# Performance work log

Measured on AMD Instinct MI355X. Metric: run time of the kernel, lower is better.

Reference implementation:

```python
import jax, jax.numpy as jnp
import numpy as np

EMBED_DIM = 2048
NUM_HEADS = 32
HEAD_DIM = EMBED_DIM // NUM_HEADS
SCALE = HEAD_DIM ** -0.5
B, S = 2, 2048


def setup_inputs() -> dict:
    key = jax.random.key(0)
    ks = jax.random.split(key, 9)
    std = EMBED_DIM ** -0.5
    inp = {
        "h": jax.random.normal(ks[0], (B, S, EMBED_DIM), dtype=jnp.float32),
        "Wq": jax.random.normal(ks[1], (EMBED_DIM, EMBED_DIM), dtype=jnp.float32) * std,
        "bq": jax.random.normal(ks[2], (EMBED_DIM,), dtype=jnp.float32) * 0.02,
        "Wk": jax.random.normal(ks[3], (EMBED_DIM, EMBED_DIM), dtype=jnp.float32) * std,
        "bk": jax.random.normal(ks[4], (EMBED_DIM,), dtype=jnp.float32) * 0.02,
        "Wv": jax.random.normal(ks[5], (EMBED_DIM, EMBED_DIM), dtype=jnp.float32) * std,
        "bv": jax.random.normal(ks[6], (EMBED_DIM,), dtype=jnp.float32) * 0.02,
        "Wo": jax.random.normal(ks[7], (EMBED_DIM, EMBED_DIM), dtype=jnp.float32) * std,
        "bo": jax.random.normal(ks[8], (EMBED_DIM,), dtype=jnp.float32) * 0.02,
    }
    return inp


def reference(h, Wq, bq, Wk, bk, Wv, bv, Wo, bo):
    # QKV projections (nn.Linear: x @ W.T + b)
    q = h @ Wq.T + bq  # [B, S, E]
    k = h @ Wk.T + bk
    v = h @ Wv.T + bv
    # split heads
    q = q.reshape(B, S, NUM_HEADS, HEAD_DIM)
    k = k.reshape(B, S, NUM_HEADS, HEAD_DIM)
    v = v.reshape(B, S, NUM_HEADS, HEAD_DIM)
    # scaled dot-product attention with causal (tril) mask
    scores = jnp.einsum("bqhd,bkhd->bhqk", q, k) * SCALE  # [B, H, S, S]
    causal = jnp.tril(jnp.ones((S, S), dtype=bool))  # [S, S]
    neg = jnp.finfo(scores.dtype).min
    scores = jnp.where(causal[None, None, :, :], scores, neg)
    attn = jax.nn.softmax(scores, axis=-1)
    o = jnp.einsum("bhqk,bkhd->bqhd", attn, v).reshape(B, S, EMBED_DIM)
    return o @ Wo.T + bo
```

## Files before the change

kernel.cpp:

```cpp
#include <hip/hip_runtime.h>
#include <hip/hip_bf16.h>
#include <stdint.h>

#define EMBED 2048
#define NHEADS 32
#define HDIM 64
#define BATCH 2
#define SEQ 2048
#define ATT_SCALE 0.125f
#define LOG2E 1.4426950408889634f

typedef __attribute__((ext_vector_type(8))) short bf16x8;
typedef __attribute__((ext_vector_type(4))) float f32x4;
typedef __attribute__((ext_vector_type(16))) float f32x16;
typedef __attribute__((ext_vector_type(4))) unsigned short u16x4;
typedef __attribute__((ext_vector_type(2))) unsigned int u32x2;

static __device__ __forceinline__ unsigned short f2bf(float f) {
  union { float f; uint32_t u; } v; v.f = f;
  uint32_t r = v.u + 0x7fffu + ((v.u >> 16) & 1u);
  return (unsigned short)(r >> 16);
}

static __device__ __forceinline__ void gload_lds16(const unsigned short* g, unsigned short* l) {
  __builtin_amdgcn_global_load_lds(
      (const __attribute__((address_space(1))) unsigned int*)g,
      (__attribute__((address_space(3))) unsigned int*)l, 16, 0, 0);
}

__global__ void cvt_all(const float* __restrict__ h,
                        const float* __restrict__ Wq, const float* __restrict__ Wk,
                        const float* __restrict__ Wv, const float* __restrict__ Wo,
                        unsigned short* __restrict__ out) {
  const int n4 = 6291456;
  int idx = blockIdx.x * blockDim.x + threadIdx.x;
  int stride = gridDim.x * blockDim.x;
  for (int i = idx; i < n4; i += stride) {
    const float* src; int off;
    if (i < 2097152)      { src = h;  off = i; }
    else if (i < 3145728) { src = Wq; off = i - 2097152; }
    else if (i < 4194304) { src = Wk; off = i - 3145728; }
    else if (i < 5242880) { src = Wv; off = i - 4194304; }
    else                  { src = Wo; off = i - 5242880; }
    float4 v = ((const float4*)src)[off];
    u16x4 o;
    o.x = f2bf(v.x); o.y = f2bf(v.y); o.z = f2bf(v.z); o.w = f2bf(v.w);
    ((u16x4*)out)[i] = o;
  }
}

__global__ __launch_bounds__(512, 2)
void gemm_qkv192(const unsigned short* __restrict__ A,
                 const unsigned short* __restrict__ W,
                 const float* __restrict__ b0, const float* __restrict__ b1,
                 const float* __restrict__ b2,
                 unsigned short* __restrict__ o0, unsigned short* __restrict__ o1,
                 unsigned short* __restrict__ o2, float qscale) {
  __shared__ unsigned short lds[2][28672];
  const int tid = threadIdx.x;
  const int w = tid >> 6, l = tid & 63;
  const int wm = w >> 2, wn = w & 3;
  const int r16 = l & 15, g = l >> 4;
  const int xcd = blockIdx.x & 7, t8 = blockIdx.x >> 3;
  const int bi = (xcd >> 2) * 8 + (t8 & 7);
  const int bj = (xcd & 3) * 8 + (t8 >> 3);
  const int arow0 = bi * 256, bcol0 = bj * 192;

  f32x4 acc[8][3];
#pragma unroll
  for (int i = 0; i < 8; ++i)
#pragma unroll
    for (int j = 0; j < 3; ++j) acc[i][j] = (f32x4){0.f, 0.f, 0.f, 0.f};

  const int lr8 = (l >> 3) & 7;
  const int gcu = ((l & 7) ^ lr8) * 8;

  auto stageA = [&](int buf, int kt, int base) {
    gload_lds16(A + (size_t)(arow0 + base + (tid >> 3)) * 2048 + kt * 64 + gcu,
                &lds[buf][(base + w * 8) * 64]);
  };
  auto stageB = [&](int buf, int kt, int k) {
    gload_lds16(W + (size_t)(bcol0 + k * 64 + (tid >> 3)) * 2048 + kt * 64 + gcu,
                &lds[buf][16384 + (k * 64 + w * 8) * 64]);
  };
  auto ldA = [&](int buf, int mf, int ks) -> bf16x8 {
    const int row = wm * 128 + mf * 16 + r16;
    const int u = (ks * 4 + g) ^ (r16 & 7);
    return *(const bf16x8*)&lds[buf][row * 64 + u * 8];
  };
  auto ldB = [&](int buf, int nf, int ks) -> bf16x8 {
    const int row = wn * 48 + nf * 16 + r16;
    const int u = (ks * 4 + g) ^ (r16 & 7);
    return *(const bf16x8*)&lds[buf][16384 + row * 64 + u * 8];
  };

  bf16x8 af[4][2], bfr[3][2];

#define MMA_H(MH)                                                                  \
  __builtin_amdgcn_s_setprio(1);                                                   \
  _Pragma("unroll")                                                                \
  for (int i = 0; i < 4; ++i)                                                      \
    _Pragma("unroll")                                                              \
    for (int j = 0; j < 3; ++j)                                                    \
      _Pragma("unroll")                                                            \
      for (int ks = 0; ks < 2; ++ks)                                               \
        acc[(MH)*4 + i][j] = __builtin_amdgcn_mfma_f32_16x16x32_bf16(              \
            af[i][ks], bfr[j][ks], acc[(MH)*4 + i][j], 0, 0, 0);                   \
  __builtin_amdgcn_s_setprio(0);

  stageB(0, 0, 0); stageB(0, 0, 1); stageB(0, 0, 2);
  stageA(0, 0, 0); stageA(0, 0, 128);
  stageA(0, 0, 64); stageA(0, 0, 192);
  asm volatile("s_waitcnt vmcnt(2)" ::: "memory");
  __builtin_amdgcn_sched_barrier(0);
  __builtin_amdgcn_s_barrier();

  const int nt = 32;
  for (int c = 0; c < nt; ++c) {
    const int X = c & 1, Y = X ^ 1;
    const bool s1 = (c + 1 < nt);
#pragma unroll
    for (int i = 0; i < 4; ++i) { af[i][0] = ldA(X, i, 0); af[i][1] = ldA(X, i, 1); }
#pragma unroll
    for (int j = 0; j < 3; ++j) { bfr[j][0] = ldB(X, j, 0); bfr[j][1] = ldB(X, j, 1); }
    if (s1) { stageB(Y, c + 1, 0); stageB(Y, c + 1, 1); stageB(Y, c + 1, 2); }
    MMA_H(0);
    __builtin_amdgcn_s_barrier();
    if (s1) asm volatile("s_waitcnt vmcnt(3)" ::: "memory");
    else    asm volatile("s_waitcnt vmcnt(0)" ::: "memory");
    __builtin_amdgcn_sched_barrier(0);
#pragma unroll
    for (int i = 0; i < 4; ++i) { af[i][0] = ldA(X, i + 4, 0); af[i][1] = ldA(X, i + 4, 1); }
    if (s1) {
      stageA(Y, c + 1, 0); stageA(Y, c + 1, 128);
      stageA(Y, c + 1, 64); stageA(Y, c + 1, 192);
    }
    MMA_H(1);
    if (s1) asm volatile("s_waitcnt vmcnt(2)" ::: "memory");
    else    asm volatile("s_waitcnt vmcnt(0)" ::: "memory");
    __builtin_amdgcn_sched_barrier(0);
    __builtin_amdgcn_s_barrier();
  }
#undef MMA_H

#pragma unroll
  for (int mf = 0; mf < 8; ++mf) {
    const int irow = arow0 + wm * 128 + mf * 16 + g * 4;
#pragma unroll
    for (int nf = 0; nf < 3; ++nf) {
      const int jcol = bcol0 + wn * 48 + nf * 16 + r16;
      const int which = jcol >> 11;
      const int jl = jcol & 2047;
      const int hh = jl >> 6, d = jl & 63;
      const float bval = (which == 0) ? b0[jl] : (which == 1) ? b1[jl] : b2[jl];
      const float osc = (which == 0) ? qscale : 1.0f;
      unsigned short* outp = (which == 0) ? o0 : (which == 1) ? o1 : o2;
#pragma unroll
      for (int rr = 0; rr < 4; ++rr) {
        const float val = (acc[mf][nf][rr] + bval) * osc;
        const int i = irow + rr;
        const int b = i >> 11, s = i & 2047;
        size_t off;
        if (which < 2) off = (((size_t)(b * NHEADS + hh)) * SEQ + s) * HDIM + d;
        else           off = (((size_t)(b * NHEADS + hh)) * HDIM + d) * SEQ + s;
        outp[off] = f2bf(val);
      }
    }
  }
}

__global__ __launch_bounds__(512, 2)
void gemm8_out(const unsigned short* __restrict__ A,
               const unsigned short* __restrict__ W,
               const float* __restrict__ bias, float* __restrict__ fo) {
  __shared__ unsigned short lds[2][24576];
  const int tid = threadIdx.x;
  const int w = tid >> 6, l = tid & 63;
  const int wm = w >> 1, wn = w & 1;
  const int r16 = l & 15, g = l >> 4;
  const int NBJ = 16, nblk = 256;
  const int swz = (blockIdx.x & 7) * (nblk >> 3) + (blockIdx.x >> 3);
  const int bi = swz / NBJ, bj = swz % NBJ;
  const int arow0 = bi * 256, bcol0 = bj * 128;

  f32x4 acc[4][4];
#pragma unroll
  for (int i = 0; i < 4; ++i)
#pragma unroll
    for (int j = 0; j < 4; ++j) acc[i][j] = (f32x4){0.f, 0.f, 0.f, 0.f};

  const int lrow = l >> 3;
  const int gcu = ((l & 7) ^ lrow) * 8;

  auto stageA = [&](int buf, int t, int mq, int call) {
    const int m = call * 8 + w;
    const int row0 = mq * 32 + (m >> 2) * 64 + (m & 3) * 8;
    gload_lds16(A + (size_t)(arow0 + row0 + lrow) * 2048 + t * 64 + gcu,
                &lds[buf][row0 * 64]);
  };
  auto stageB = [&](int buf, int t, int nq) {
    const int row0 = nq * 32 + (w >> 2) * 64 + (w & 3) * 8;
    gload_lds16(W + (size_t)(bcol0 + row0 + lrow) * 2048 + t * 64 + gcu,
                &lds[buf][16384 + row0 * 64]);
  };
  auto ldA = [&](int buf, int mf, int ks) -> bf16x8 {
    const int row = wm * 64 + mf * 16 + r16;
    const int u = (ks * 4 + g) ^ (r16 & 7);
    return *(const bf16x8*)&lds[buf][row * 64 + u * 8];
  };
  auto ldB = [&](int buf, int nf, int ks) -> bf16x8 {
    const int row = wn * 64 + nf * 16 + r16;
    const int u = (ks * 4 + g) ^ (r16 & 7);
    return *(const bf16x8*)&lds[buf][16384 + row * 64 + u * 8];
  };

  stageA(0, 0, 0, 0); stageA(0, 0, 0, 1); stageB(0, 0, 0);
  stageA(0, 0, 1, 0); stageA(0, 0, 1, 1); stageB(0, 0, 1);
  stageA(1, 1, 0, 0); stageA(1, 1, 0, 1); stageB(1, 1, 0);
  asm volatile("s_waitcnt vmcnt(3)" ::: "memory");
  __builtin_amdgcn_sched_barrier(0);
  __builtin_amdgcn_s_barrier();

  bf16x8 af[2][2], bfr[4][2];

#define MMA_Q(MQ, NQ)                                                          \
  __builtin_amdgcn_s_setprio(1);                                               \
  _Pragma("unroll")                                                            \
  for (int i = 0; i < 2; ++i)                                                  \
    _Pragma("unroll")                                                          \
    for (int j = 0; j < 2; ++j)                                                \
      _Pragma("unroll")                                                        \
      for (int ks = 0; ks < 2; ++ks)                                           \
        acc[(MQ)*2 + i][(NQ)*2 + j] = __builtin_amdgcn_mfma_f32_16x16x32_bf16( \
            af[i][ks], bfr[(NQ)*2 + j][ks], acc[(MQ)*2 + i][(NQ)*2 + j], 0, 0, 0); \
  __builtin_amdgcn_s_setprio(0);

  const int nt = 32;
  for (int c = 0; c < nt; ++c) {
    const int X = c & 1;
    const bool s1 = (c + 1 < nt), s2 = (c + 2 < nt);
    af[0][0] = ldA(X, 0, 0); af[0][1] = ldA(X, 0, 1);
    af[1][0] = ldA(X, 1, 0); af[1][1] = ldA(X, 1, 1);
    bfr[0][0] = ldB(X, 0, 0); bfr[0][1] = ldB(X, 0, 1);
    bfr[1][0] = ldB(X, 1, 0); bfr[1][1] = ldB(X, 1, 1);
    if (s1) { stageA(X ^ 1, c + 1, 1, 0); stageA(X ^ 1, c + 1, 1, 1); }
    MMA_Q(0, 0);
    __builtin_amdgcn_s_barrier();
    bfr[2][0] = ldB(X, 2, 0); bfr[2][1] = ldB(X, 2, 1);
    bfr[3][0] = ldB(X, 3, 0); bfr[3][1] = ldB(X, 3, 1);
    if (s1) stageB(X ^ 1, c + 1, 1);
    MMA_Q(0, 1);
    __builtin_amdgcn_s_barrier();
    af[0][0] = ldA(X, 2, 0); af[0][1] = ldA(X, 2, 1);
    af[1][0] = ldA(X, 3, 0); af[1][1] = ldA(X, 3, 1);
    if (s2) { stageA(X, c + 2, 0, 0); stageA(X, c + 2, 0, 1); }
    MMA_Q(1, 0);
    __builtin_amdgcn_s_barrier();
    if (s2) stageB(X, c + 2, 0);
    MMA_Q(1, 1);
    if (s2) asm volatile("s_waitcnt vmcnt(3)" ::: "memory");
    else    asm volatile("s_waitcnt vmcnt(0)" ::: "memory");
    __builtin_amdgcn_sched_barrier(0);
    __builtin_amdgcn_s_barrier();
  }
#undef MMA_Q

#pragma unroll
  for (int mf = 0; mf < 4; ++mf) {
    const int irow = arow0 + wm * 64 + mf * 16 + g * 4;
#pragma unroll
    for (int nf = 0; nf < 4; ++nf) {
      const int jcol = bcol0 + wn * 64 + nf * 16 + r16;
      const float bval = bias[jcol];
#pragma unroll
      for (int rr = 0; rr < 4; ++rr)
        fo[(size_t)(irow + rr) * 2048 + jcol] = acc[mf][nf][rr] + bval;
    }
  }
}

__global__ __launch_bounds__(256, 2)
void attn_kernel(const unsigned short* __restrict__ Q,
                 const unsigned short* __restrict__ K,
                 const unsigned short* __restrict__ Vt,
                 unsigned short* __restrict__ O) {
  __shared__ unsigned short K_lds[2][64 * 72];
  __shared__ unsigned short V_lds[2][64 * 72];
  __shared__ __align__(16) float abuf[4][32];
  __shared__ __align__(16) float lbuf[4][32];
  const int tid = threadIdx.x;
  const int w = tid >> 6, l = tid & 63;
  const int q5 = l & 31, hi = l >> 5;
  const int bid = ((blockIdx.x & 7) << 6) | (blockIdx.x >> 3);
  const int pair = bid & 7;
  const int bh = bid >> 3;
  const unsigned short* Qh = Q + (size_t)bh * SEQ * HDIM;
  const unsigned short* Kh = K + (size_t)bh * SEQ * HDIM;
  const unsigned short* Vh = Vt + (size_t)bh * HDIM * SEQ;
  const int bq = bh >> 5, hh = bh & 31;
  const int srow = tid >> 3;
  const int scol = (tid & 7) * 8;

  for (int half = 0; half < 2; ++half) {
    const int qt = half ? (15 - pair) : pair;
    const int wrow0 = qt * 128 + w * 32;
    const int wrow_max = wrow0 + 31;
    const int n_tiles = 2 * qt + 2;
    const int qrow = wrow0 + q5;

    bf16x8 qf[4];
#pragma unroll
    for (int ks = 0; ks < 4; ++ks)
      qf[ks] = *(const bf16x8*)(Qh + (size_t)qrow * HDIM + ks * 16 + hi * 8);

    f32x16 oacc[2];
#pragma unroll
    for (int df = 0; df < 2; ++df)
#pragma unroll
      for (int r = 0; r < 16; ++r) oacc[df][r] = 0.f;
    float m_run = -3.0e38f, l_run = 0.f;

    bf16x8 kreg[2], vreg[2];
#pragma unroll
    for (int j = 0; j < 2; ++j) {
      const int rr = j * 32 + srow;
      kreg[j] = *(const bf16x8*)(Kh + (size_t)rr * HDIM + scol);
      vreg[j] = *(const bf16x8*)(Vh + (size_t)rr * SEQ + scol);
    }
    __syncthreads();
#pragma unroll
    for (int j = 0; j < 2; ++j) {
      const int rr = j * 32 + srow;
      *(bf16x8*)(K_lds[0] + rr * 72 + scol) = kreg[j];
      *(bf16x8*)(V_lds[0] + rr * 72 + scol) = vreg[j];
    }

    for (int t = 0; t < n_tiles; ++t) {
      const int cur = t & 1;
      const bool not_last = (t + 1 < n_tiles);
      if (not_last) {
#pragma unroll
        for (int j = 0; j < 2; ++j) {
          const int rr = j * 32 + srow;
          kreg[j] = *(const bf16x8*)(Kh + (size_t)((t + 1) * 64 + rr) * HDIM + scol);
          vreg[j] = *(const bf16x8*)(Vh + (size_t)rr * SEQ + (t + 1) * 64 + scol);
        }
      }
      __syncthreads();

      if (t * 64 <= wrow_max) {
        f32x16 skf[2];
#pragma unroll
        for (int kf = 0; kf < 2; ++kf)
#pragma unroll
          for (int r = 0; r < 16; ++r) skf[kf][r] = 0.f;
        __builtin_amdgcn_s_setprio(1);
#pragma unroll
        for (int kf = 0; kf < 2; ++kf)
#pragma unroll
          for (int ks = 0; ks < 4; ++ks) {
            bf16x8 ak = *(const bf16x8*)(K_lds[cur] + (kf * 32 + q5) * 72 + ks * 16 + hi * 8);
            skf[kf] = __builtin_amdgcn_mfma_f32_32x32x16_bf16(ak, qf[ks], skf[kf], 0, 0, 0);
          }
        __builtin_amdgcn_s_setprio(0);

        const bool need_mask = (t * 64 + 63 > wrow0);
        if (need_mask) {
#pragma unroll
          for (int kf = 0; kf < 2; ++kf)
#pragma unroll
            for (int r = 0; r < 16; ++r) {
              const int key = t * 64 + kf * 32 + (r & 3) + 8 * (r >> 2) + 4 * hi;
              if (key > qrow) skf[kf][r] = -3.0e38f;
            }
        }

        float mx = -3.0e38f;
#pragma unroll
        for (int kf = 0; kf < 2; ++kf)
#pragma unroll
          for (int r = 0; r < 16; ++r) mx = fmaxf(mx, skf[kf][r]);
        mx = fmaxf(mx, __shfl_xor(mx, 32));

        if (__any(mx > m_run + 8.0f)) {
          const float mnew = fmaxf(m_run, mx);
          const float alpha = exp2f(m_run - mnew);
          m_run = mnew;
          l_run *= alpha;
          if (l < 32) abuf[w][l] = alpha;
          f32x4 av[4];
#pragma unroll
          for (int k = 0; k < 4; ++k)
            av[k] = *(const f32x4*)&abuf[w][8 * k + 4 * hi];
#pragma unroll
          for (int df = 0; df < 2; ++df)
#pragma unroll
            for (int r = 0; r < 16; ++r) oacc[df][r] *= av[r >> 2][r & 3];
        }

        unsigned int pkA[8], pkB[8];
        float psum = 0.f;
#pragma unroll
        for (int kf = 0; kf < 2; ++kf)
#pragma unroll
          for (int rr = 0; rr < 4; ++rr) {
            unsigned int pb[4];
#pragma unroll
            for (int j = 0; j < 4; ++j) {
              const float p = exp2f(skf[kf][rr * 4 + j] - m_run);
              psum += p;
              union { float f; unsigned int u; } c; c.f = p;
              pb[j] = c.u + 0x8000u;
            }
            pkA[kf * 4 + rr] = __builtin_amdgcn_perm(pb[1], pb[0], 0x07060302);
            pkB[kf * 4 + rr] = __builtin_amdgcn_perm(pb[3], pb[2], 0x07060302);
          }
        psum += __shfl_xor(psum, 32);
        l_run += psum;

        __builtin_amdgcn_s_setprio(1);
#pragma unroll
        for (int ks = 0; ks < 4; ++ks) {
          u32x2 ra = __builtin_amdgcn_permlane32_swap(pkA[2 * ks], pkA[2 * ks + 1], false, false);
          u32x2 rb = __builtin_amdgcn_permlane32_swap(pkB[2 * ks], pkB[2 * ks + 1], false, false);
          union { unsigned int u[4]; bf16x8 v; } pa;
          pa.u[0] = ra.x; pa.u[1] = rb.x; pa.u[2] = ra.y; pa.u[3] = rb.y;
#pragma unroll
          for (int df = 0; df < 2; ++df) {
            bf16x8 vf = *(const bf16x8*)(V_lds[cur] + (df * 32 + q5) * 72 + ks * 16 + hi * 8);
            oacc[df] = __builtin_amdgcn_mfma_f32_32x32x16_bf16(pa.v, vf, oacc[df], 0, 0, 0);
          }
        }
        __builtin_amdgcn_s_setprio(0);
      }

      if (not_last) {
#pragma unroll
        for (int j = 0; j < 2; ++j) {
          const int rr = j * 32 + srow;
          *(bf16x8*)(K_lds[cur ^ 1] + rr * 72 + scol) = kreg[j];
          *(bf16x8*)(V_lds[cur ^ 1] + rr * 72 + scol) = vreg[j];
        }
      }
    }

    if (l < 32) lbuf[w][l] = l_run;
    f32x4 lv[4];
#pragma unroll
    for (int k = 0; k < 4; ++k)
      lv[k] = *(const f32x4*)&lbuf[w][8 * k + 4 * hi];
#pragma unroll
    for (int df = 0; df < 2; ++df) {
      const int d = df * 32 + q5;
#pragma unroll
      for (int r = 0; r < 16; ++r) {
        const int s = wrow0 + (r & 3) + 8 * (r >> 2) + 4 * hi;
        const float inv = __builtin_amdgcn_rcpf(lv[r >> 2][r & 3]);
        O[((size_t)(bq * SEQ + s)) * EMBED + hh * HDIM + d] = f2bf(oacc[df][r] * inv);
      }
    }
  }
}

extern "C" void kernel_launch(void* const* d_in, const int* in_sizes, int n_in,
                              void* d_out, int out_size, void* d_ws, size_t ws_size,
                              hipStream_t stream) {
  const float* h  = (const float*)d_in[0];
  const float* Wq = (const float*)d_in[1];
  const float* bq = (const float*)d_in[2];
  const float* Wk = (const float*)d_in[3];
  const float* bk = (const float*)d_in[4];
  const float* Wv = (const float*)d_in[5];
  const float* bv = (const float*)d_in[6];
  const float* Wo = (const float*)d_in[7];
  const float* bo = (const float*)d_in[8];

  if (ws_size < (size_t)117440512) return;

  unsigned short* ws = (unsigned short*)d_ws;
  unsigned short* hb = ws;
  unsigned short* wqb = ws + 8388608;
  unsigned short* wob = ws + 20971520;
  unsigned short* Qw  = ws + 25165824;
  unsigned short* Kw  = ws + 33554432;
  unsigned short* Vw  = ws + 41943040;
  unsigned short* Ow  = ws + 50331648;

  cvt_all<<<2048, 256, 0, stream>>>(h, Wq, Wk, Wv, Wo, ws);

  const float qscale = ATT_SCALE * LOG2E;
  gemm_qkv192<<<512, 512, 0, stream>>>(hb, wqb, bq, bk, bv, Qw, Kw, Vw, qscale);

  attn_kernel<<<512, 256, 0, stream>>>(Qw, Kw, Vw, Ow);

  gemm8_out<<<256, 512, 0, stream>>>(Ow, wob, bo, (float*)d_out);
}
```

Measured before the change: 249.4 us.

## Load QKV GEMM weight fragments directly from global into registers, bypassing LDS

The QKV projection GEMM no longer stages the weight (B) tile through shared memory. Each wave now loads its B fragments straight from global memory into double-buffered registers that are prefetched one k-step ahead. LDS drops to A-only buffers, and the loop is unrolled by two so the register buffers can ping-pong. This removes the LDS write/read traffic for B and some LDS capacity pressure, at the cost of uncoalesced-ish global loads for B, duplicated reads across waves sharing wn, and extra register pressure.

```diff
diff --git a/kernel.cpp b/kernel.cpp
--- a/kernel.cpp
+++ b/kernel.cpp
@@ -50,13 +50,13 @@
 }
 
 __global__ __launch_bounds__(512, 2)
-void gemm_qkv192(const unsigned short* __restrict__ A,
+void gemm_qkv_bd(const unsigned short* __restrict__ A,
                  const unsigned short* __restrict__ W,
                  const float* __restrict__ b0, const float* __restrict__ b1,
                  const float* __restrict__ b2,
                  unsigned short* __restrict__ o0, unsigned short* __restrict__ o1,
                  unsigned short* __restrict__ o2, float qscale) {
-  __shared__ unsigned short lds[2][28672];
+  __shared__ unsigned short lds[2][16384];
   const int tid = threadIdx.x;
   const int w = tid >> 6, l = tid & 63;
   const int wm = w >> 2, wn = w & 3;
@@ -72,80 +72,86 @@
 #pragma unroll
     for (int j = 0; j < 3; ++j) acc[i][j] = (f32x4){0.f, 0.f, 0.f, 0.f};
 
-  const int lr8 = (l >> 3) & 7;
-  const int gcu = ((l & 7) ^ lr8) * 8;
+  const int gcu = ((l & 7) ^ ((l >> 3) & 7)) * 8;
 
   auto stageA = [&](int buf, int kt, int base) {
     gload_lds16(A + (size_t)(arow0 + base + (tid >> 3)) * 2048 + kt * 64 + gcu,
                 &lds[buf][(base + w * 8) * 64]);
   };
-  auto stageB = [&](int buf, int kt, int k) {
-    gload_lds16(W + (size_t)(bcol0 + k * 64 + (tid >> 3)) * 2048 + kt * 64 + gcu,
-                &lds[buf][16384 + (k * 64 + w * 8) * 64]);
-  };
-  auto ldA = [&](int buf, int mf, int ks) -> bf16x8 {
-    const int row = wm * 128 + mf * 16 + r16;
+  auto ldA = [&](int buf, int half, int mf, int ks) -> bf16x8 {
+    const int row = wm * 128 + half * 64 + mf * 16 + r16;
     const int u = (ks * 4 + g) ^ (r16 & 7);
     return *(const bf16x8*)&lds[buf][row * 64 + u * 8];
   };
-  auto ldB = [&](int buf, int nf, int ks) -> bf16x8 {
-    const int row = wn * 48 + nf * 16 + r16;
-    const int u = (ks * 4 + g) ^ (r16 & 7);
-    return *(const bf16x8*)&lds[buf][16384 + row * 64 + u * 8];
-  };
-
-  bf16x8 af[4][2], bfr[3][2];
-
-#define MMA_H(MH)                                                                  \
-  __builtin_amdgcn_s_setprio(1);                                                   \
-  _Pragma("unroll")                                                                \
-  for (int i = 0; i < 4; ++i)                                                      \
-    _Pragma("unroll")                                                              \
-    for (int j = 0; j < 3; ++j)                                                    \
-      _Pragma("unroll")                                                            \
-      for (int ks = 0; ks < 2; ++ks)                                               \
-        acc[(MH)*4 + i][j] = __builtin_amdgcn_mfma_f32_16x16x32_bf16(              \
-            af[i][ks], bfr[j][ks], acc[(MH)*4 + i][j], 0, 0, 0);                   \
+  auto ldBg = [&](int kt, int j, int ks) -> bf16x8 {
+    return *(const bf16x8*)(W + (size_t)(bcol0 + wn * 48 + j * 16 + r16) * 2048 +
+                            kt * 64 + ks * 32 + g * 8);
+  };
+
+  bf16x8 af[4][2], bA[3][2], bB[3][2];
+
+#define MMA_H(MH, BREG)                                                        \
+  __builtin_amdgcn_s_setprio(1);                                               \
+  _Pragma("unroll")                                                            \
+  for (int mf = 0; mf < 4; ++mf)                                               \
+    _Pragma("unroll")                                                          \
+    for (int j = 0; j < 3; ++j)                                                \
+      _Pragma("unroll")                                                        \
+      for (int ks = 0; ks < 2; ++ks)                                           \
+        acc[(MH)*4 + mf][j] = __builtin_amdgcn_mfma_f32_16x16x32_bf16(         \
+            af[mf][ks], BREG[j][ks], acc[(MH)*4 + mf][j], 0, 0, 0);            \
   __builtin_amdgcn_s_setprio(0);
 
-  stageB(0, 0, 0); stageB(0, 0, 1); stageB(0, 0, 2);
-  stageA(0, 0, 0); stageA(0, 0, 128);
+#define ITER(c, X, BCUR, BNXT, S1)                                             \
+  {                                                                            \
+                                      \
+    _Pragma("unroll")                                                          \
+    for (int mf = 0; mf < 4; ++mf) {                                           \
+      af[mf][0] = ldA(X, 0, mf, 0); af[mf][1] = ldA(X, 0, mf, 1); }            \
+    MMA_H(0, BCUR);                                                            \
+    asm volatile("s_waitcnt vmcnt(0)" ::: "memory");                           \
+    __builtin_amdgcn_sched_barrier(0);                                         \
+    __builtin_amdgcn_s_barrier();                                              \
+      \
+    _Pragma("unroll")                                                          \
+    for (int mf = 0; mf < 4; ++mf) {                                           \
+      af[mf][0] = ldA(X, 1, mf, 0); af[mf][1] = ldA(X, 1, mf, 1); }            \
+    if (S1) {                                                                  \
+      _Pragma("unroll")                                                        \
+      for (int j2 = 0; j2 < 3; ++j2) {                                         \
+        BNXT[j2][0] = ldBg((c) + 1, j2, 0);                                    \
+        BNXT[j2][1] = ldBg((c) + 1, j2, 1); }                                  \
+      stageA((X) ^ 1, (c) + 1, 0);  stageA((X) ^ 1, (c) + 1, 128);             \
+      stageA((X) ^ 1, (c) + 1, 64); stageA((X) ^ 1, (c) + 1, 192);             \
+    }                                                                          \
+    MMA_H(1, BCUR);                                                            \
+    if (S1) asm volatile("s_waitcnt vmcnt(2)" ::: "memory");                   \
+    else    asm volatile("s_waitcnt vmcnt(0)" ::: "memory");                   \
+    __builtin_amdgcn_sched_barrier(0);                                         \
+    __builtin_amdgcn_s_barrier();                                              \
+  }
+
+#pragma unroll
+  for (int j2 = 0; j2 < 3; ++j2) {
+    bA[j2][0] = ldBg(0, j2, 0);
+    bA[j2][1] = ldBg(0, j2, 1);
+  }
+  stageA(0, 0, 0);  stageA(0, 0, 128);
   stageA(0, 0, 64); stageA(0, 0, 192);
   asm volatile("s_waitcnt vmcnt(2)" ::: "memory");
   __builtin_amdgcn_sched_barrier(0);
   __builtin_amdgcn_s_barrier();
 
-  const int nt = 32;
-  for (int c = 0; c < nt; ++c) {
-    const int X = c & 1, Y = X ^ 1;
-    const bool s1 = (c + 1 < nt);
-#pragma unroll
-    for (int i = 0; i < 4; ++i) { af[i][0] = ldA(X, i, 0); af[i][1] = ldA(X, i, 1); }
-#pragma unroll
-    for (int j = 0; j < 3; ++j) { bfr[j][0] = ldB(X, j, 0); bfr[j][1] = ldB(X, j, 1); }
-    if (s1) { stageB(Y, c + 1, 0); stageB(Y, c + 1, 1); stageB(Y, c + 1, 2); }
-    MMA_H(0);
-    __builtin_amdgcn_s_barrier();
-    if (s1) asm volatile("s_waitcnt vmcnt(3)" ::: "memory");
-    else    asm volatile("s_waitcnt vmcnt(0)" ::: "memory");
-    __builtin_amdgcn_sched_barrier(0);
-#pragma unroll
-    for (int i = 0; i < 4; ++i) { af[i][0] = ldA(X, i + 4, 0); af[i][1] = ldA(X, i + 4, 1); }
-    if (s1) {
-      stageA(Y, c + 1, 0); stageA(Y, c + 1, 128);
-      stageA(Y, c + 1, 64); stageA(Y, c + 1, 192);
-    }
-    MMA_H(1);
-    if (s1) asm volatile("s_waitcnt vmcnt(2)" ::: "memory");
-    else    asm volatile("s_waitcnt vmcnt(0)" ::: "memory");
-    __builtin_amdgcn_sched_barrier(0);
-    __builtin_amdgcn_s_barrier();
-  }
+  for (int c = 0; c < 32; c += 2) {
+    ITER(c, 0, bA, bB, true);
+    ITER(c + 1, 1, bB, bA, (c + 1 < 31));
+  }
+#undef ITER
 #undef MMA_H
 
 #pragma unroll
   for (int mf = 0; mf < 8; ++mf) {
-    const int irow = arow0 + wm * 128 + mf * 16 + g * 4;
+    const int irow = arow0 + wm * 128 + ((mf & 1) ? 64 : 0) + (mf >> 1) * 16 + g * 4;
 #pragma unroll
     for (int nf = 0; nf < 3; ++nf) {
       const int jcol = bcol0 + wn * 48 + nf * 16 + r16;
@@ -155,9 +161,10 @@
       const float bval = (which == 0) ? b0[jl] : (which == 1) ? b1[jl] : b2[jl];
       const float osc = (which == 0) ? qscale : 1.0f;
       unsigned short* outp = (which == 0) ? o0 : (which == 1) ? o1 : o2;
+      const int ai = ((mf & 1) ? 4 : 0) + (mf >> 1);
 #pragma unroll
       for (int rr = 0; rr < 4; ++rr) {
-        const float val = (acc[mf][nf][rr] + bval) * osc;
+        const float val = (acc[ai][nf][rr] + bval) * osc;
         const int i = irow + rr;
         const int b = i >> 11, s = i & 2047;
         size_t off;
@@ -489,7 +496,7 @@
   cvt_all<<<2048, 256, 0, stream>>>(h, Wq, Wk, Wv, Wo, ws);
 
   const float qscale = ATT_SCALE * LOG2E;
-  gemm_qkv192<<<512, 512, 0, stream>>>(hb, wqb, bq, bk, bv, Qw, Kw, Vw, qscale);
+  gemm_qkv_bd<<<512, 512, 0, stream>>>(hb, wqb, bq, bk, bv, Qw, Kw, Vw, qscale);
 
   attn_kernel<<<512, 256, 0, stream>>>(Qw, Kw, Vw, Ow);
 
```

After: 313.4 us. 1.26x slower.
